# Kernel optimization log

Hardware: AMD Instinct MI355X
Metric: run time of the kernel (lower is better)

The kernel has to match this reference:

```python
import jax, jax.numpy as jnp
import numpy as np
import math

B, L, D = 2, 2048, 1024
H, HD = 16, 64          # num heads, head dim
R = 256                 # kv lora rank = D // 4
E, K, F = 8, 2, 1024    # routed experts, top_k, intermediate size


def rmsnorm(x, w, eps=1e-6):
    ms = jnp.mean(x * x, axis=-1, keepdims=True)
    return w * (x * jax.lax.rsqrt(ms + eps))


def setup_inputs() -> dict:
    key = jax.random.key(0)
    ks = jax.random.split(key, 16)
    s = 0.02
    return {
        "x": jax.random.normal(ks[0], (B, L, D), jnp.float32),
        "ln1_w": jnp.ones((D,), jnp.float32),
        "q_w": jax.random.normal(ks[1], (D, H * HD), jnp.float32) * s,
        "kvd_w": jax.random.normal(ks[2], (D, R), jnp.float32) * s,
        "kvn_w": jnp.ones((R,), jnp.float32),
        "kvu_w": jax.random.normal(ks[3], (R, 2 * H * HD), jnp.float32) * s,
        "o_w": jax.random.normal(ks[4], (H * HD, D), jnp.float32) * s,
        "ln2_w": jnp.ones((D,), jnp.float32),
        "gate_w": jax.random.normal(ks[5], (D, E), jnp.float32) * s,
        "sh_w1": jax.random.normal(ks[6], (D, F), jnp.float32) * s,
        "sh_w2": jax.random.normal(ks[7], (F, D), jnp.float32) * s,
        "sh_w3": jax.random.normal(ks[8], (D, F), jnp.float32) * s,
        "re_w1": jax.random.normal(ks[9], (E, D, F), jnp.float32) * s,
        "re_w2": jax.random.normal(ks[10], (E, F, D), jnp.float32) * s,
        "re_w3": jax.random.normal(ks[11], (E, D, F), jnp.float32) * s,
    }


def reference(x, ln1_w, q_w, kvd_w, kvn_w, kvu_w, o_w, ln2_w, gate_w,
              sh_w1, sh_w2, sh_w3, re_w1, re_w2, re_w3):
    # ---- MLHA attention with pre-RMSNorm and latent-compressed KV ----
    xn = rmsnorm(x, ln1_w)
    q = (xn @ q_w).reshape(B, L, H, HD)
    latent = rmsnorm(xn @ kvd_w, kvn_w)                 # [B,L,R]
    kv = latent @ kvu_w                                 # [B,L,2*H*HD]
    k, v = jnp.split(kv, 2, axis=-1)
    k = k.reshape(B, L, H, HD)
    v = v.reshape(B, L, H, HD)
    scores = jnp.einsum('bxhd,byhd->bhxy', q, k) / math.sqrt(HD)
    causal = jnp.tril(jnp.ones((L, L), bool))
    scores = jnp.where(causal, scores, -jnp.inf)
    attn = jax.nn.softmax(scores, axis=-1)
    attn_out = jnp.einsum('bhxy,byhd->bxhd', attn, v).reshape(B, L, H * HD)
    h = x + attn_out @ o_w

    # ---- MoE (inference: no jitter, expert_bias = 0, no bias update) ----
    hn = rmsnorm(h, ln2_w)
    flat = hn.reshape(-1, D)                            # [T,D], T=B*L
    # shared expert (SwiGLU)
    shared = (jax.nn.silu(flat @ sh_w1) * (flat @ sh_w3)) @ sh_w2
    # router
    logits = flat @ gate_w                              # [T,E]
    probs = jax.nn.softmax(logits, axis=-1)
    topw, topi = jax.lax.top_k(probs, K)                # [T,K]
    topw = topw / jnp.sum(topw, axis=-1, keepdims=True)
    # per-token per-expert combine weight [T,E]
    combine = jnp.sum(topw[..., None] * jax.nn.one_hot(topi, E, dtype=flat.dtype), axis=1)
    # all routed experts densely, then masked combine (same math as masked loop)
    h1 = jnp.einsum('td,edf->etf', flat, re_w1)
    h3 = jnp.einsum('td,edf->etf', flat, re_w3)
    eo = jnp.einsum('etf,efd->etd', jax.nn.silu(h1) * h3, re_w2)
    routed = jnp.einsum('te,etd->td', combine, eo)
    moe_out = (shared + routed).reshape(B, L, D)
    return h + moe_out, probs
```

## Files before the change

### kernel.cpp

```cpp
#include <hip/hip_runtime.h>
#include <hip/hip_bf16.h>
#include <cstdint>
#include <cstddef>

typedef unsigned short u16;
typedef unsigned int u32;
typedef __attribute__((ext_vector_type(8))) short bf16x8;
typedef __attribute__((ext_vector_type(4))) float f32x4;

static constexpr int Bb = 2, Ll = 2048, Dd = 1024, Hh = 16, Rr = 256, Ee = 8, Ff = 1024;
static constexpr int Tt = Bb * Ll;
static constexpr float QSCALE = 0.18033688011112042f;

__device__ __forceinline__ u16 f2bf(float f){
  union { float f; u32 u; } v; v.f = f;
  u32 u = v.u;
  u32 r = u + 0x7FFFu + ((u >> 16) & 1u);
  return (u16)(r >> 16);
}
__device__ __forceinline__ float bf2f(u16 b){
  union { u32 u; float f; } v; v.u = ((u32)b) << 16; return v.f;
}

#define GLDS(gp, lp) __builtin_amdgcn_global_load_lds( \
    (const __attribute__((address_space(1))) unsigned int*)(gp), \
    (__attribute__((address_space(3))) unsigned int*)(lp), 16, 0, 0)

__global__ void transpose5(const float* __restrict__ q_w, const float* __restrict__ o_w,
                           const float* __restrict__ w1, const float* __restrict__ w3,
                           const float* __restrict__ w2,
                           u16* __restrict__ qkvdT, u16* __restrict__ oT,
                           u16* __restrict__ sh13T, u16* __restrict__ sh2T){
  const float* s; u16* d; int off, str;
  switch (blockIdx.z){
    case 0: s = q_w; d = qkvdT; off = 0; str = 1; break;
    case 1: s = o_w; d = oT;    off = 0; str = 1; break;
    case 2: s = w1;  d = sh13T; off = 0; str = 2; break;
    case 3: s = w3;  d = sh13T; off = 1; str = 2; break;
    default: s = w2; d = sh2T;  off = 0; str = 1; break;
  }
  __shared__ float tile[32][33];
  int bx = blockIdx.x * 32, by = blockIdx.y * 32;
  int tx = threadIdx.x, ty = threadIdx.y;
  #pragma unroll
  for (int i = ty; i < 32; i += 8) tile[i][tx] = s[(size_t)(by + i) * 1024 + bx + tx];
  __syncthreads();
  #pragma unroll
  for (int i = ty; i < 32; i += 8)
    d[(size_t)(off + (bx + i) * str) * 1024 + by + tx] = f2bf(tile[tx][i]);
}

__global__ void transposeEx(const float* __restrict__ re_w1, const float* __restrict__ re_w3,
                            const float* __restrict__ re_w2,
                            u16* __restrict__ re13T, u16* __restrict__ re2T){
  int z = blockIdx.z, which = z >> 3, e = z & 7;
  const float* s; u16* d; int off, str;
  size_t eo = (size_t)e * 1024 * 1024;
  if (which == 0){ s = re_w1 + eo; d = re13T + (size_t)e * 2048 * 1024; off = 0; str = 2; }
  else if (which == 1){ s = re_w3 + eo; d = re13T + (size_t)e * 2048 * 1024; off = 1; str = 2; }
  else { s = re_w2 + eo; d = re2T + (size_t)e * 1024 * 1024; off = 0; str = 1; }
  __shared__ float tile[32][33];
  int bx = blockIdx.x * 32, by = blockIdx.y * 32;
  int tx = threadIdx.x, ty = threadIdx.y;
  #pragma unroll
  for (int i = ty; i < 32; i += 8) tile[i][tx] = s[(size_t)(by + i) * 1024 + bx + tx];
  __syncthreads();
  #pragma unroll
  for (int i = ty; i < 32; i += 8)
    d[(size_t)(off + (bx + i) * str) * 1024 + by + tx] = f2bf(tile[tx][i]);
}

__global__ void transpose_conv(const float* __restrict__ src, u16* __restrict__ dst,
                               int K, int N, int dstOff){
  __shared__ float tile[32][33];
  int bx = blockIdx.x * 32, by = blockIdx.y * 32;
  int tx = threadIdx.x, ty = threadIdx.y;
  #pragma unroll
  for (int i = ty; i < 32; i += 8) tile[i][tx] = src[(size_t)(by + i) * N + bx + tx];
  __syncthreads();
  #pragma unroll
  for (int i = ty; i < 32; i += 8)
    dst[(size_t)(dstOff + bx + i) * K + by + tx] = f2bf(tile[tx][i]);
}

template<int DIM>
__global__ void rmsnorm_kernel(const float* __restrict__ x, const float* __restrict__ w,
                               u16* __restrict__ out){
  int t = blockIdx.x;
  const float* xr = x + (size_t)t * DIM;
  u16* orow = out + (size_t)t * DIM;
  int tid = threadIdx.x;
  constexpr int NT = 256;
  constexpr int PER = DIM / NT > 0 ? DIM / NT : 1;
  float vals[PER];
  float ss = 0.f;
  #pragma unroll
  for (int i = 0; i < PER; i++){
    int d = tid + i * NT;
    float v = (d < DIM) ? xr[d] : 0.f;
    vals[i] = v; ss += v * v;
  }
  __shared__ float red[4];
  for (int m = 32; m; m >>= 1) ss += __shfl_xor(ss, m, 64);
  if ((tid & 63) == 0) red[tid >> 6] = ss;
  __syncthreads();
  float tot = red[0] + red[1] + red[2] + red[3];
  float rn = rsqrtf(tot / DIM + 1e-6f);
  #pragma unroll
  for (int i = 0; i < PER; i++){
    int d = tid + i * NT;
    if (d < DIM) orow[d] = f2bf(vals[i] * rn * w[d]);
  }
}

__global__ void router_kernel(const float* __restrict__ h, const float* __restrict__ ln2w,
                              const float* __restrict__ gate,
                              float* __restrict__ probs_out,
                              int* __restrict__ topi, float* __restrict__ topw,
                              u16* __restrict__ hn){
  int t = blockIdx.x; int tid = threadIdx.x;
  const float* hr = h + (size_t)t * Dd;
  float v[4]; float ss = 0.f;
  #pragma unroll
  for (int i = 0; i < 4; i++){ float x = hr[tid + i * 256]; v[i] = x; ss += x * x; }
  __shared__ float red[4];
  for (int m = 32; m; m >>= 1) ss += __shfl_xor(ss, m, 64);
  if ((tid & 63) == 0) red[tid >> 6] = ss;
  __syncthreads();
  float rn = rsqrtf((red[0] + red[1] + red[2] + red[3]) / Dd + 1e-6f);
  float p[8];
  #pragma unroll
  for (int e = 0; e < 8; e++) p[e] = 0.f;
  #pragma unroll
  for (int i = 0; i < 4; i++){
    int d = tid + i * 256;
    float hv = v[i] * rn * ln2w[d];
    hn[(size_t)t * Dd + d] = f2bf(hv);
    const float* g = gate + (size_t)d * 8;
    #pragma unroll
    for (int e = 0; e < 8; e++) p[e] += hv * g[e];
  }
  #pragma unroll
  for (int e = 0; e < 8; e++){
    float x = p[e];
    for (int m = 32; m; m >>= 1) x += __shfl_xor(x, m, 64);
    p[e] = x;
  }
  __shared__ float pe[4][8];
  if ((tid & 63) == 0){ for (int e = 0; e < 8; e++) pe[tid >> 6][e] = p[e]; }
  __syncthreads();
  if (tid == 0){
    float lg[8];
    for (int e = 0; e < 8; e++) lg[e] = pe[0][e] + pe[1][e] + pe[2][e] + pe[3][e];
    float mx = lg[0];
    for (int e = 1; e < 8; e++) mx = fmaxf(mx, lg[e]);
    float pr[8]; float s = 0.f;
    for (int e = 0; e < 8; e++){ pr[e] = __expf(lg[e] - mx); s += pr[e]; }
    float inv = 1.f / s;
    for (int e = 0; e < 8; e++) probs_out[(size_t)t * 8 + e] = pr[e] * inv;
    int i0 = 0;
    for (int e = 1; e < 8; e++) if (pr[e] > pr[i0]) i0 = e;
    int i1 = -1;
    for (int e = 0; e < 8; e++){ if (e == i0) continue; if (i1 < 0 || pr[e] > pr[i1]) i1 = e; }
    float w0 = pr[i0], w1 = pr[i1]; float wn = 1.f / (w0 + w1);
    topi[t * 2] = i0; topi[t * 2 + 1] = i1;
    topw[t * 2] = w0 * wn; topw[t * 2 + 1] = w1 * wn;
  }
}

__global__ void hist_kernel(const int* __restrict__ topi, int* __restrict__ counts){
  __shared__ int h[8];
  int tid = threadIdx.x;
  if (tid < 8) h[tid] = 0;
  __syncthreads();
  int base = blockIdx.x * 512;
  for (int i = tid; i < 512; i += 256) atomicAdd(&h[topi[base + i]], 1);
  __syncthreads();
  if (tid < 8) atomicAdd(&counts[tid], h[tid]);
}

__global__ void bucket_kernel(const int* __restrict__ topi, const float* __restrict__ topw,
                              const int* __restrict__ counts, int* __restrict__ cur,
                              int* __restrict__ entries, float* __restrict__ ew){
  __shared__ int lh[8], lbase[8], lcur[8], loffs[8];
  int tid = threadIdx.x;
  if (tid < 8) lh[tid] = 0;
  __syncthreads();
  int t = blockIdx.x * 256 + tid;
  int e0 = topi[t * 2], e1 = topi[t * 2 + 1];
  atomicAdd(&lh[e0], 1); atomicAdd(&lh[e1], 1);
  __syncthreads();
  if (tid == 0){
    int c = 0;
    for (int e = 0; e < 8; e++){ loffs[e] = c; c += counts[e]; }
  }
  if (tid < 8){ lbase[tid] = atomicAdd(&cur[tid], lh[tid]); lcur[tid] = 0; }
  __syncthreads();
  int p0 = atomicAdd(&lcur[e0], 1);
  int pos0 = loffs[e0] + lbase[e0] + p0;
  entries[pos0] = t; ew[pos0] = topw[t * 2];
  int p1 = atomicAdd(&lcur[e1], 1);
  int pos1 = loffs[e1] + lbase[e1] + p1;
  entries[pos1] = t; ew[pos1] = topw[t * 2 + 1];
}

template<int TM, int ROWMODE, int MODE>
__launch_bounds__(256)
__global__ void gemm_bt(const u16* __restrict__ A, const u16* __restrict__ Bt,
                        void* __restrict__ C, const float* __restrict__ res,
                        int M, int N, int K, int lda, int ldc,
                        const int* __restrict__ entries, const float* __restrict__ ew,
                        const int* __restrict__ counts,
                        float* __restrict__ outAt){
  constexpr int MTC = TM / 32;
  __shared__ __align__(16) u16 As[TM * 32];
  __shared__ __align__(16) u16 Bs[128 * 32];
  __shared__ int els[TM];
  __shared__ float ewl[TM];

  int e = (ROWMODE ? blockIdx.z : 0);
  const u16* Bte = Bt + (size_t)e * N * K;
  int cnt, off;
  if (ROWMODE == 0){ cnt = M; off = 0; }
  else {
    cnt = counts[e];
    off = 0;
    for (int i = 0; i < e; i++) off += counts[i];
  }
  int rt = blockIdx.y * TM;
  if (rt >= cnt) return;
  int cb = blockIdx.x * 128;
  int tid = threadIdx.x;

  if (ROWMODE >= 1){
    if (tid < TM){
      int r = rt + tid;
      els[tid] = (r < cnt) ? entries[off + r] : 0;
      ewl[tid] = (MODE == 4 && r < cnt) ? ew[off + r] : 0.f;
    }
    __syncthreads();
  }

  int sr = tid >> 2;
  int skc = (tid & 3) * 8;
  int rr0 = rt + sr, rr1 = rt + sr + 64;
  size_t ar0 = 0, ar1 = 0;
  if (ROWMODE == 0){ ar0 = (size_t)rr0; ar1 = (size_t)rr1; }
  else if (ROWMODE == 1){ ar0 = (size_t)els[sr];
                          ar1 = (TM == 128) ? (size_t)els[sr + 64] : 0; }
  else {
    int c0 = rr0 < cnt ? rr0 : (cnt - 1);
    int c1 = rr1 < cnt ? rr1 : (cnt - 1);
    ar0 = (size_t)off + c0; ar1 = (size_t)off + c1;
  }
  const u16* pa0 = A + ar0 * lda + skc;
  const u16* pa1 = A + ar1 * lda + skc;
  const u16* pb0 = Bte + (size_t)(cb + sr) * K + skc;
  const u16* pb1 = Bte + (size_t)(cb + sr + 64) * K + skc;
  u16* lA0 = &As[tid * 8];
  u16* lA1 = &As[(TM == 128 ? 2048 : 0) + tid * 8];
  u16* lB0 = &Bs[tid * 8];
  u16* lB1 = &Bs[2048 + tid * 8];

  int w = tid >> 6, lane = tid & 63;
  int wm = w >> 1, wn = w & 1;
  int quad = lane >> 4, l16 = lane & 15;

  f32x4 acc[MTC][4];
  const f32x4 zf = {0.f, 0.f, 0.f, 0.f};
  #pragma unroll
  for (int i = 0; i < MTC; i++)
    #pragma unroll
    for (int j = 0; j < 4; j++) acc[i][j] = zf;

  for (int k0 = 0; k0 < K; k0 += 32){
    __syncthreads();
    GLDS(pa0 + k0, lA0);
    if (TM == 128) GLDS(pa1 + k0, lA1);
    GLDS(pb0 + k0, lB0);
    GLDS(pb1 + k0, lB1);
    __syncthreads();
    bf16x8 af[MTC], bfr[4];
    #pragma unroll
    for (int mt = 0; mt < MTC; mt++)
      af[mt] = *(const bf16x8*)&As[(wm * (TM / 2) + mt * 16 + l16) * 32 + quad * 8];
    #pragma unroll
    for (int nt = 0; nt < 4; nt++)
      bfr[nt] = *(const bf16x8*)&Bs[(wn * 64 + nt * 16 + l16) * 32 + quad * 8];
    #pragma unroll
    for (int mt = 0; mt < MTC; mt++)
      #pragma unroll
      for (int nt = 0; nt < 4; nt++)
        acc[mt][nt] = __builtin_amdgcn_mfma_f32_16x16x32_bf16(af[mt], bfr[nt], acc[mt][nt], 0, 0, 0);
  }

  #pragma unroll
  for (int mt = 0; mt < MTC; mt++){
    #pragma unroll
    for (int nt = 0; nt < 4; nt++){
      #pragma unroll
      for (int r = 0; r < 4; r++){
        int row = wm * (TM / 2) + mt * 16 + quad * 4 + r;
        int col = cb + wn * 64 + nt * 16 + l16;
        int rr = rt + row;
        float v = acc[mt][nt][r];
        if (MODE == 6){
          float pv = __shfl_xor(v, 1, 64);
          if (rr < cnt && (l16 & 1) == 0){
            float sl = v / (1.f + __expf(-v));
            size_t crow = (size_t)((ROWMODE == 1) ? (off + rr) : rr);
            ((u16*)C)[crow * ldc + (col >> 1)] = f2bf(sl * pv);
          }
          continue;
        }
        if (rr >= cnt) continue;
        if (MODE == 0){
          size_t ci = (size_t)((ROWMODE == 1) ? (off + rr) : rr) * ldc + col;
          ((u16*)C)[ci] = f2bf(v);
        } else if (MODE == 1){
          size_t ci = (size_t)rr * ldc + col;
          ((float*)C)[ci] = v + res[ci];
        } else if (MODE == 5){
          if (col < 1024) ((u16*)C)[(size_t)rr * 1024 + col] = f2bf(v * QSCALE);
          else            outAt[(size_t)rr * 256 + (col - 1024)] = v;
        } else {
          int tok = els[row];
          atomicAdd(&outAt[(size_t)tok * ldc + col], ewl[row] * v);
        }
      }
    }
  }
}

#define RBAR() __builtin_amdgcn_s_barrier()
#define MMQ(MQ, NQ, FA, FB) do{ \
  _Pragma("unroll") \
  for (int m4_ = 0; m4_ < 4; m4_++){ \
    _Pragma("unroll") \
    for (int n2_ = 0; n2_ < 2; n2_++){ \
      acc[(MQ)*4+m4_][(NQ)*2+n2_] = __builtin_amdgcn_mfma_f32_16x16x32_bf16(FA[m4_][0], FB[n2_][0], acc[(MQ)*4+m4_][(NQ)*2+n2_], 0, 0, 0); \
      acc[(MQ)*4+m4_][(NQ)*2+n2_] = __builtin_amdgcn_mfma_f32_16x16x32_bf16(FA[m4_][1], FB[n2_][1], acc[(MQ)*4+m4_][(NQ)*2+n2_], 0, 0, 0); \
    } \
  } }while(0)
#define RDA(DST, BB, MQ) do{ \
  _Pragma("unroll") \
  for (int m4_ = 0; m4_ < 4; m4_++){ \
    const char* p_ = (const char*)(&As[BB][0]) + (size_t)(wm*128 + (MQ)*64 + m4_*16 + l16)*128; \
    DST[m4_][0] = *(const bf16x8*)(p_ + offk0); \
    DST[m4_][1] = *(const bf16x8*)(p_ + offk1); \
  } }while(0)
#define RDB(DST, BB, NQ) do{ \
  _Pragma("unroll") \
  for (int n2_ = 0; n2_ < 2; n2_++){ \
    const char* p_ = (const char*)(&Bs[BB][0]) + (size_t)(wn*64 + (NQ)*32 + n2_*16 + l16)*128; \
    DST[n2_][0] = *(const bf16x8*)(p_ + offk0); \
    DST[n2_][1] = *(const bf16x8*)(p_ + offk1); \
  } }while(0)
#define STGA(SB, H, KT) do{ \
  GLDS(gA[(H)*2+0] + (size_t)(KT)*64, &As[SB][((H)*128 +  0)*64] + (size_t)tid*8); \
  GLDS(gA[(H)*2+1] + (size_t)(KT)*64, &As[SB][((H)*128 + 64)*64] + (size_t)tid*8); }while(0)
#define STGB(SB, H, KT) do{ \
  GLDS(gB[(H)*2+0] + (size_t)(KT)*64, &Bs[SB][((H)*128 +  0)*64] + (size_t)tid*8); \
  GLDS(gB[(H)*2+1] + (size_t)(KT)*64, &Bs[SB][((H)*128 + 64)*64] + (size_t)tid*8); }while(0)

__launch_bounds__(512, 2)
__global__ void gemm256_up(const u16* __restrict__ A,
                           const u16* __restrict__ sh13, const u16* __restrict__ re13,
                           u16* __restrict__ shg, u16* __restrict__ gr,
                           const int* __restrict__ entries, const int* __restrict__ counts){
  __shared__ __align__(16) u16 As[2][256 * 64];
  __shared__ __align__(16) u16 Bs[2][256 * 64];

  int e = blockIdx.z;
  int cnt, off = 0;
  if (e < 8){
    cnt = counts[e];
    for (int i = 0; i < e; i++) off += counts[i];
  } else cnt = Tt;
  int rt = blockIdx.y * 256;
  if (rt >= cnt) return;
  int cb = blockIdx.x * 256;
  const u16* Bte = (e < 8) ? (re13 + (size_t)e * 2048 * 1024) : sh13;
  u16* Cb = (e < 8) ? gr : shg;

  int tid = threadIdx.x;
  int w = tid >> 6, lane = tid & 63, quad = lane >> 4, l16 = lane & 15;
  int wm = w >> 2, wn = w & 3;
  int swz = (l16 & 7) << 4;
  int offk0 = (quad * 16) ^ swz;
  int offk1 = (64 + quad * 16) ^ swz;

  int trow = tid >> 3;
  int sk = ((((tid & 7) << 4) ^ ((trow & 7) << 4)) >> 1);
  const u16* gA[4]; const u16* gB[4];
  #pragma unroll
  for (int i = 0; i < 4; i++){
    int r = i * 64 + trow;
    int garow;
    if (e < 8){
      int idx = rt + r; if (idx >= cnt) idx = cnt - 1;
      garow = entries[off + idx];
    } else garow = rt + r;
    gA[i] = A + (size_t)garow * 1024 + sk;
    gB[i] = Bte + (size_t)(cb + r) * 1024 + sk;
  }

  f32x4 acc[8][4];
  const f32x4 zf = {0.f, 0.f, 0.f, 0.f};
  #pragma unroll
  for (int i = 0; i < 8; i++)
    #pragma unroll
    for (int j = 0; j < 4; j++) acc[i][j] = zf;

  STGB(0, 0, 0); STGB(0, 1, 0);
  STGA(0, 0, 0); STGA(0, 1, 0);
  __syncthreads();

  bf16x8 fa0[4][2], fa1[4][2], fb0[2][2], fb1[2][2];

  for (int it = 0; it < 8; ++it){
    int t1 = 2 * it + 1, t2 = 2 * it + 2;
    RDA(fa0, 0, 0); RDB(fb0, 0, 0);
    STGB(1, 0, t1);
    RBAR();
    __builtin_amdgcn_s_setprio(1); MMQ(0, 0, fa0, fb0); __builtin_amdgcn_s_setprio(0);
    RBAR();

    RDB(fb1, 0, 1);
    STGB(1, 1, t1);
    RBAR();
    __builtin_amdgcn_s_setprio(1); MMQ(0, 1, fa0, fb1); __builtin_amdgcn_s_setprio(0);
    RBAR();

    RDA(fa1, 0, 1);
    STGA(1, 0, t1);
    RBAR();
    __builtin_amdgcn_s_setprio(1); MMQ(1, 0, fa1, fb0); __builtin_amdgcn_s_setprio(0);
    RBAR();

    STGA(1, 1, t1);
    RBAR();
    __builtin_amdgcn_s_setprio(1); MMQ(1, 1, fa1, fb1); __builtin_amdgcn_s_setprio(0);
    __syncthreads();

    bool pf = (it < 7);
    RDA(fa0, 1, 0); RDB(fb0, 1, 0);
    if (pf) STGB(0, 0, t2);
    RBAR();
    __builtin_amdgcn_s_setprio(1); MMQ(0, 0, fa0, fb0); __builtin_amdgcn_s_setprio(0);
    RBAR();

    RDB(fb1, 1, 1);
    if (pf) STGB(0, 1, t2);
    RBAR();
    __builtin_amdgcn_s_setprio(1); MMQ(0, 1, fa0, fb1); __builtin_amdgcn_s_setprio(0);
    RBAR();

    RDA(fa1, 1, 1);
    if (pf) STGA(0, 0, t2);
    RBAR();
    __builtin_amdgcn_s_setprio(1); MMQ(1, 0, fa1, fb0); __builtin_amdgcn_s_setprio(0);
    RBAR();

    if (pf) STGA(0, 1, t2);
    RBAR();
    __builtin_amdgcn_s_setprio(1); MMQ(1, 1, fa1, fb1); __builtin_amdgcn_s_setprio(0);
    __syncthreads();
  }

  #pragma unroll
  for (int mi = 0; mi < 8; mi++){
    #pragma unroll
    for (int ni = 0; ni < 4; ni++){
      #pragma unroll
      for (int r = 0; r < 4; r++){
        int row = wm * 128 + (mi >> 2) * 64 + (mi & 3) * 16 + quad * 4 + r;
        int col = cb + wn * 64 + (ni >> 1) * 32 + (ni & 1) * 16 + l16;
        float v = acc[mi][ni][r];
        float pv = __shfl_xor(v, 1, 64);
        int grow = rt + row;
        if (grow < cnt && (l16 & 1) == 0){
          float sl = v / (1.f + __expf(-v));
          size_t crow = (e < 8) ? (size_t)(off + grow) : (size_t)grow;
          Cb[crow * 1024 + (col >> 1)] = f2bf(sl * pv);
        }
      }
    }
  }
}

__global__ void vt_kernel(const u16* __restrict__ kv, u16* __restrict__ vt){
  __shared__ __align__(16) u16 t[64 * 72];
  int kt = blockIdx.x * 64, h = blockIdx.y, b = blockIdx.z;
  size_t bL = (size_t)b * Ll;
  int tid = threadIdx.x;
  int r = tid >> 2, c0 = (tid & 3) * 16;
  const u16* src = kv + (bL + kt + r) * 2048 + 1024 + h * 64 + c0;
  *(uint4*)&t[r * 72 + c0]     = *(const uint4*)(src);
  *(uint4*)&t[r * 72 + c0 + 8] = *(const uint4*)(src + 8);
  __syncthreads();
  int d = tid >> 2; int k0 = (tid & 3) * 16;
  u16 tmp[16];
  #pragma unroll
  for (int j = 0; j < 16; j++) tmp[j] = t[(k0 + j) * 72 + d];
  u16* dst = vt + ((size_t)(b * Hh + h) * 64 + d) * (size_t)Ll + kt + k0;
  *(uint4*)dst       = *(const uint4*)&tmp[0];
  *(uint4*)(dst + 8) = *(const uint4*)&tmp[8];
}

__launch_bounds__(256)
__global__ void attn_kernel(const u16* __restrict__ q, const u16* __restrict__ kv,
                            const u16* __restrict__ vt, u16* __restrict__ out){
  constexpr int LD = 72;
  __shared__ __align__(16) u16 Ks[2][64 * LD];
  __shared__ __align__(16) u16 Vs[2][64 * LD];
  __shared__ __align__(16) u16 Ps[64 * LD];
  int h = blockIdx.y, b = blockIdx.z;
  size_t bL = (size_t)b * Ll;
  int tid = threadIdx.x, w = tid >> 6, lane = tid & 63, quad = lane >> 4, l16 = lane & 15;
  int sr = tid >> 2, sc = (tid & 3) * 16;
  const u16* kbase = kv + (bL + sr) * 2048 + h * 64 + sc;
  const u16* vbase = vt + ((size_t)(b * Hh + h) * 64 + sr) * (size_t)Ll + sc;
  const f32x4 zf = {0.f, 0.f, 0.f, 0.f};

  #pragma unroll
  for (int pass = 0; pass < 2; pass++){
    int q0 = (pass ? (31 - (int)blockIdx.x) : (int)blockIdx.x) * 64;
    int qrow = q0 + w * 16 + l16;

    bf16x8 qf[2];
    #pragma unroll
    for (int ks = 0; ks < 2; ks++)
      qf[ks] = *(const bf16x8*)(q + (bL + qrow) * 1024 + h * 64 + ks * 32 + quad * 8);

    f32x4 oacc[4];
    #pragma unroll
    for (int dt = 0; dt < 4; dt++) oacc[dt] = zf;
    float mprev = -1e30f, lsum = 0.f;

    uint4 kr0 = *(const uint4*)(kbase);
    uint4 kr1 = *(const uint4*)(kbase + 8);
    uint4 vr0 = *(const uint4*)(vbase);
    uint4 vr1 = *(const uint4*)(vbase + 8);
    *(uint4*)&Ks[0][sr * LD + sc]     = kr0;
    *(uint4*)&Ks[0][sr * LD + sc + 8] = kr1;
    *(uint4*)&Vs[0][sr * LD + sc]     = vr0;
    *(uint4*)&Vs[0][sr * LD + sc + 8] = vr1;
    int cur = 0;
    __syncthreads();

    for (int kt = 0; kt <= q0; kt += 64){
      bool pfetch = (kt + 64 <= q0);
      if (pfetch){
        const u16* kp = kbase + (size_t)(kt + 64) * 2048;
        kr0 = *(const uint4*)(kp);
        kr1 = *(const uint4*)(kp + 8);
        const u16* vp = vbase + kt + 64;
        vr0 = *(const uint4*)(vp);
        vr1 = *(const uint4*)(vp + 8);
      }
      const u16* ksp = Ks[cur];
      const u16* vsp = Vs[cur];

      f32x4 sacc[4];
      #pragma unroll
      for (int mt = 0; mt < 4; mt++) sacc[mt] = zf;
      __builtin_amdgcn_s_setprio(1);
      #pragma unroll
      for (int ks = 0; ks < 2; ks++){
        #pragma unroll
        for (int mt = 0; mt < 4; mt++){
          bf16x8 kf = *(const bf16x8*)&ksp[(mt * 16 + l16) * LD + ks * 32 + quad * 8];
          sacc[mt] = __builtin_amdgcn_mfma_f32_16x16x32_bf16(kf, qf[ks], sacc[mt], 0, 0, 0);
        }
      }
      __builtin_amdgcn_s_setprio(0);

      bool diag = (kt == q0);
      int lq = w * 16 + l16;
      float sv[16]; float mx = -1e30f;
      #pragma unroll
      for (int mt = 0; mt < 4; mt++){
        #pragma unroll
        for (int r = 0; r < 4; r++){
          float s = sacc[mt][r];
          if (diag && (mt * 16 + quad * 4 + r > lq)) s = -1e30f;
          sv[mt * 4 + r] = s;
          mx = fmaxf(mx, s);
        }
      }
      mx = fmaxf(mx, __shfl_xor(mx, 16, 64));
      mx = fmaxf(mx, __shfl_xor(mx, 32, 64));
      if (!__all(mx <= mprev)){
        float mnew = fmaxf(mprev, mx);
        float alpha = exp2f(mprev - mnew);
        mprev = mnew;
        lsum *= alpha;
        #pragma unroll
        for (int dt = 0; dt < 4; dt++) oacc[dt] *= alpha;
      }
      float rs = 0.f;
      #pragma unroll
      for (int mt = 0; mt < 4; mt++){
        float p0 = exp2f(sv[mt * 4 + 0] - mprev);
        float p1 = exp2f(sv[mt * 4 + 1] - mprev);
        float p2 = exp2f(sv[mt * 4 + 2] - mprev);
        float p3 = exp2f(sv[mt * 4 + 3] - mprev);
        rs += p0 + p1 + p2 + p3;
        union { uint2 u; __hip_bfloat162 h2[2]; } pk;
        pk.h2[0] = __float22bfloat162_rn(make_float2(p0, p1));
        pk.h2[1] = __float22bfloat162_rn(make_float2(p2, p3));
        *(uint2*)&Ps[(w * 16 + l16) * LD + mt * 16 + quad * 4] = pk.u;
      }
      rs += __shfl_xor(rs, 16, 64);
      rs += __shfl_xor(rs, 32, 64);
      lsum += rs;

      __builtin_amdgcn_s_setprio(1);
      #pragma unroll
      for (int ks = 0; ks < 2; ks++){
        bf16x8 pfr = *(const bf16x8*)&Ps[(w * 16 + l16) * LD + ks * 32 + quad * 8];
        #pragma unroll
        for (int dt = 0; dt < 4; dt++){
          bf16x8 vf = *(const bf16x8*)&vsp[(dt * 16 + l16) * LD + ks * 32 + quad * 8];
          oacc[dt] = __builtin_amdgcn_mfma_f32_16x16x32_bf16(vf, pfr, oacc[dt], 0, 0, 0);
        }
      }
      __builtin_amdgcn_s_setprio(0);

      if (pfetch){
        int nb = cur ^ 1;
        *(uint4*)&Ks[nb][sr * LD + sc]     = kr0;
        *(uint4*)&Ks[nb][sr * LD + sc + 8] = kr1;
        *(uint4*)&Vs[nb][sr * LD + sc]     = vr0;
        *(uint4*)&Vs[nb][sr * LD + sc + 8] = vr1;
        cur = nb;
      }
      __syncthreads();
    }

    float inv = 1.f / lsum;
    #pragma unroll
    for (int dt = 0; dt < 4; dt++){
      union { uint2 u; __hip_bfloat162 h2[2]; } ov;
      ov.h2[0] = __float22bfloat162_rn(make_float2(oacc[dt][0] * inv, oacc[dt][1] * inv));
      ov.h2[1] = __float22bfloat162_rn(make_float2(oacc[dt][2] * inv, oacc[dt][3] * inv));
      *(uint2*)(out + (bL + qrow) * 1024 + h * 64 + dt * 16 + quad * 4) = ov.u;
    }
  }
}

extern "C" void kernel_launch(void* const* d_in, const int* in_sizes, int n_in,
                              void* d_out, int out_size, void* d_ws, size_t ws_size,
                              hipStream_t stream){
  const float* x     = (const float*)d_in[0];
  const float* ln1_w = (const float*)d_in[1];
  const float* q_w   = (const float*)d_in[2];
  const float* kvd_w = (const float*)d_in[3];
  const float* kvn_w = (const float*)d_in[4];
  const float* kvu_w = (const float*)d_in[5];
  const float* o_w   = (const float*)d_in[6];
  const float* ln2_w = (const float*)d_in[7];
  const float* gate_w= (const float*)d_in[8];
  const float* sh_w1 = (const float*)d_in[9];
  const float* sh_w2 = (const float*)d_in[10];
  const float* sh_w3 = (const float*)d_in[11];
  const float* re_w1 = (const float*)d_in[12];
  const float* re_w2 = (const float*)d_in[13];
  const float* re_w3 = (const float*)d_in[14];
  float* out = (float*)d_out;

  char* wp = (char*)d_ws;
  auto alloc = [&](size_t bytes)->char*{
    char* p = wp; wp += (bytes + 255) & ~(size_t)255; return p;
  };
  u16* qkvdT = (u16*)alloc((size_t)1280 * 1024 * 2);
  u16* kvuT  = (u16*)alloc((size_t)2048 * 256 * 2);
  u16* oT    = (u16*)alloc((size_t)1024 * 1024 * 2);
  u16* sh13T = (u16*)alloc((size_t)2048 * 1024 * 2);
  u16* sh2T  = (u16*)alloc((size_t)1024 * 1024 * 2);
  u16* re13T = (u16*)alloc((size_t)8 * 2048 * 1024 * 2);
  u16* re2T  = (u16*)alloc((size_t)8 * 1024 * 1024 * 2);
  u16* xn    = (u16*)alloc((size_t)Tt * 1024 * 2);
  u16* qbuf  = (u16*)alloc((size_t)Tt * 1024 * 2);
  float* latpre = (float*)alloc((size_t)Tt * 256 * 4);
  u16* lat   = (u16*)alloc((size_t)Tt * 256 * 2);
  u16* kvbuf = (u16*)alloc((size_t)Tt * 2048 * 2);
  u16* attnb = (u16*)alloc((size_t)Tt * 1024 * 2);
  float* hbuf = (float*)alloc((size_t)Tt * 1024 * 4);
  u16* vtb   = (u16*)alloc((size_t)Bb * Hh * 64 * Ll * 2);
  u16* gr    = (u16*)alloc((size_t)Tt * 2 * 1024 * 2);
  int* counts = (int*)alloc(32);
  int* cur    = (int*)alloc(32);
  int* topi   = (int*)alloc((size_t)Tt * 2 * 4);
  float* topw = (float*)alloc((size_t)Tt * 2 * 4);
  int* entries= (int*)alloc((size_t)Tt * 2 * 4);
  float* ewt  = (float*)alloc((size_t)Tt * 2 * 4);
  (void)ws_size; (void)n_in; (void)in_sizes; (void)out_size;

  hipMemsetAsync(counts, 0, 32, stream);
  hipMemsetAsync(cur, 0, 32, stream);

  dim3 tb(32, 8);
  transpose5<<<dim3(32, 32, 5), tb, 0, stream>>>(q_w, o_w, sh_w1, sh_w3, sh_w2,
                                                 qkvdT, oT, sh13T, sh2T);
  transpose_conv<<<dim3(8, 32, 1), tb, 0, stream>>>(kvd_w, qkvdT, 1024, 256, 1024);
  transpose_conv<<<dim3(64, 8, 1), tb, 0, stream>>>(kvu_w, kvuT, 256, 2048, 0);
  transposeEx<<<dim3(32, 32, 24), tb, 0, stream>>>(re_w1, re_w3, re_w2, re13T, re2T);

  rmsnorm_kernel<1024><<<Tt, 256, 0, stream>>>(x, ln1_w, xn);

  gemm_bt<64,0,5><<<dim3(10, 64), 256, 0, stream>>>(xn, qkvdT, qbuf, nullptr,
      Tt, 1280, 1024, 1024, 1024, nullptr, nullptr, nullptr, latpre);
  rmsnorm_kernel<256><<<Tt, 256, 0, stream>>>(latpre, kvn_w, lat);
  gemm_bt<128,0,0><<<dim3(16, 32), 256, 0, stream>>>(lat, kvuT, kvbuf, nullptr,
      Tt, 2048, 256, 256, 2048, nullptr, nullptr, nullptr, nullptr);
  vt_kernel<<<dim3(32, 16, 2), 256, 0, stream>>>(kvbuf, vtb);
  attn_kernel<<<dim3(16, 16, 2), 256, 0, stream>>>(qbuf, kvbuf, vtb, attnb);
  gemm_bt<64,0,1><<<dim3(8, 64), 256, 0, stream>>>(attnb, oT, hbuf, x,
      Tt, 1024, 1024, 1024, 1024, nullptr, nullptr, nullptr, nullptr);
  router_kernel<<<Tt, 256, 0, stream>>>(hbuf, ln2_w, gate_w, out + (size_t)Tt * Dd,
                                        topi, topw, xn);
  hist_kernel<<<16, 256, 0, stream>>>(topi, counts);
  bucket_kernel<<<16, 256, 0, stream>>>(topi, topw, counts, cur, entries, ewt);

  gemm256_up<<<dim3(8, 16, 9), 512, 0, stream>>>(xn, sh13T, re13T, kvbuf, gr,
                                                 entries, counts);

  gemm_bt<64,0,1><<<dim3(8, 64), 256, 0, stream>>>(kvbuf, sh2T, out, hbuf,
      Tt, 1024, 1024, 1024, 1024, nullptr, nullptr, nullptr, nullptr);
  gemm_bt<128,2,4><<<dim3(8, 32, 8), 256, 0, stream>>>(gr, re2T, nullptr, nullptr,
      Tt, 1024, 1024, 1024, 1024, entries, ewt, counts, out);
}
```

Measured before the change: 548.9 us.

## Deepen expert GEMM pipeline with prefetch-two-ahead and explicit vmcnt waits

Restructures the double-buffered expert GEMM main loop so global-to-LDS loads for tile t+2 are issued into the buffer just consumed, with two tiles in flight. Explicit s_waitcnt vmcnt(8) waits only on the older tile's loads instead of a full __syncthreads drain each half-iteration. The goal is to hide global memory latency behind MFMA work. It relies on the exact count of outstanding loads per tile and on barrier ordering to avoid LDS read/write races.

Result: no change. 551.1 us (+0.4%).

```diff
diff --git a/kernel.cpp b/kernel.cpp
--- a/kernel.cpp
+++ b/kernel.cpp
@@ -333,6 +333,10 @@
 }
 
 #define RBAR() __builtin_amdgcn_s_barrier()
+#define VMCNT8() do{ asm volatile("s_waitcnt vmcnt(8)" ::: "memory"); \
+                     __builtin_amdgcn_sched_barrier(0); }while(0)
+#define VMCNT0() do{ asm volatile("s_waitcnt vmcnt(0)" ::: "memory"); \
+                     __builtin_amdgcn_sched_barrier(0); }while(0)
 #define MMQ(MQ, NQ, FA, FB) do{ \
   _Pragma("unroll") \
   for (int m4_ = 0; m4_ < 4; m4_++){ \
@@ -412,61 +416,38 @@
     #pragma unroll
     for (int j = 0; j < 4; j++) acc[i][j] = zf;
 
-  STGB(0, 0, 0); STGB(0, 1, 0);
-  STGA(0, 0, 0); STGA(0, 1, 0);
-  __syncthreads();
-
-  bf16x8 fa0[4][2], fa1[4][2], fb0[2][2], fb1[2][2];
-
-  for (int it = 0; it < 8; ++it){
-    int t1 = 2 * it + 1, t2 = 2 * it + 2;
-    RDA(fa0, 0, 0); RDB(fb0, 0, 0);
-    STGB(1, 0, t1);
+  auto tile = [&](int b, int t2, bool stg){
+    bf16x8 fa0[4][2], fa1[4][2], fb0[2][2], fb1[2][2];
+    RDA(fa0, b, 0); RDB(fb0, b, 0);
     RBAR();
     __builtin_amdgcn_s_setprio(1); MMQ(0, 0, fa0, fb0); __builtin_amdgcn_s_setprio(0);
     RBAR();
-
-    RDB(fb1, 0, 1);
-    STGB(1, 1, t1);
+    RDB(fb1, b, 1);
     RBAR();
     __builtin_amdgcn_s_setprio(1); MMQ(0, 1, fa0, fb1); __builtin_amdgcn_s_setprio(0);
     RBAR();
-
-    RDA(fa1, 0, 1);
-    STGA(1, 0, t1);
+    RDA(fa1, b, 1);
     RBAR();
     __builtin_amdgcn_s_setprio(1); MMQ(1, 0, fa1, fb0); __builtin_amdgcn_s_setprio(0);
     RBAR();
-
-    STGA(1, 1, t1);
+    if (stg){ STGB(b, 0, t2); STGB(b, 1, t2); STGA(b, 0, t2); STGA(b, 1, t2); }
+    __builtin_amdgcn_s_setprio(1); MMQ(1, 1, fa1, fb1); __builtin_amdgcn_s_setprio(0);
+  };
+
+  STGB(0, 0, 0); STGB(0, 1, 0); STGA(0, 0, 0); STGA(0, 1, 0);
+  STGB(1, 0, 1); STGB(1, 1, 1); STGA(1, 0, 1); STGA(1, 1, 1);
+  VMCNT8();
+  RBAR();
+
+  for (int t = 0; t < 14; ++t){
+    tile(t & 1, t + 2, true);
+    VMCNT8();
     RBAR();
-    __builtin_amdgcn_s_setprio(1); MMQ(1, 1, fa1, fb1); __builtin_amdgcn_s_setprio(0);
-    __syncthreads();
-
-    bool pf = (it < 7);
-    RDA(fa0, 1, 0); RDB(fb0, 1, 0);
-    if (pf) STGB(0, 0, t2);
-    RBAR();
-    __builtin_amdgcn_s_setprio(1); MMQ(0, 0, fa0, fb0); __builtin_amdgcn_s_setprio(0);
-    RBAR();
-
-    RDB(fb1, 1, 1);
-    if (pf) STGB(0, 1, t2);
-    RBAR();
-    __builtin_amdgcn_s_setprio(1); MMQ(0, 1, fa0, fb1); __builtin_amdgcn_s_setprio(0);
-    RBAR();
-
-    RDA(fa1, 1, 1);
-    if (pf) STGA(0, 0, t2);
-    RBAR();
-    __builtin_amdgcn_s_setprio(1); MMQ(1, 0, fa1, fb0); __builtin_amdgcn_s_setprio(0);
-    RBAR();
-
-    if (pf) STGA(0, 1, t2);
-    RBAR();
-    __builtin_amdgcn_s_setprio(1); MMQ(1, 1, fa1, fb1); __builtin_amdgcn_s_setprio(0);
-    __syncthreads();
-  }
+  }
+  tile(0, 0, false);
+  VMCNT0();
+  RBAR();
+  tile(1, 0, false);
 
   #pragma unroll
   for (int mi = 0; mi < 8; mi++){
```
